# Optimization experiments

Measured on AMD Instinct MI355X. Metric: run time of the kernel, lower is better.

The kernel has to match this reference:

```python
import jax, jax.numpy as jnp
import numpy as np

COND = 128  # mask = first 128 dims are condition (True); last 128 are transformed


def _mlp(h, W1, b1, W2, b2, W3, b3):
    h = jax.nn.relu(h @ W1 + b1)
    h = jax.nn.relu(h @ W2 + b2)
    return h @ W3 + b3


def setup_inputs() -> dict:
    key = jax.random.key(0)
    ks = jax.random.split(key, 8)
    B, D, H, T = 65536, 256, 512, 128
    s = 0.02  # small init so exp(tanh(s_vals)) is well-behaved
    inp = {
        "x": jax.random.normal(ks[0], (B, D), dtype=jnp.float32),
        "Ws1": jax.random.normal(ks[1], (COND, H), dtype=jnp.float32) * s,
        "bs1": jnp.zeros((H,), jnp.float32),
        "Ws2": jax.random.normal(ks[2], (H, H), dtype=jnp.float32) * s,
        "bs2": jnp.zeros((H,), jnp.float32),
        "Ws3": jax.random.normal(ks[3], (H, T), dtype=jnp.float32) * s,
        "bs3": jnp.zeros((T,), jnp.float32),
        "Wt1": jax.random.normal(ks[4], (COND, H), dtype=jnp.float32) * s,
        "bt1": jnp.zeros((H,), jnp.float32),
        "Wt2": jax.random.normal(ks[5], (H, H), dtype=jnp.float32) * s,
        "bt2": jnp.zeros((H,), jnp.float32),
        "Wt3": jax.random.normal(ks[6], (H, T), dtype=jnp.float32) * s,
        "bt3": jnp.zeros((T,), jnp.float32),
    }
    return inp


def reference(x, Ws1, bs1, Ws2, bs2, Ws3, bs3, Wt1, bt1, Wt2, bt2, Wt3, bt3):
    # mask gather: condition = masked dims, transform = the rest
    cond = x[:, :COND]            # [B, COND]
    x_t = x[:, COND:]             # [B, T]
    s_vals = jnp.tanh(_mlp(cond, Ws1, bs1, Ws2, bs2, Ws3, bs3))  # [B, T]
    t_vals = _mlp(cond, Wt1, bt1, Wt2, bt2, Wt3, bt3)            # [B, T]
    y_partial = x_t * jnp.exp(s_vals) + t_vals                   # forward branch (inverse=False)
    log_det = s_vals.sum(axis=1)                                 # [B]
    y = jnp.concatenate([cond, y_partial], axis=1)               # scatter back
    return (y, log_det)
```

## Files before the change

kernel.cpp:

```cpp
#include <hip/hip_runtime.h>
#include <hip/hip_bf16.h>

typedef __bf16          bf16x8_t __attribute__((ext_vector_type(8)));
typedef float           f32x4_t  __attribute__((ext_vector_type(4)));
typedef unsigned short  u16x4_t  __attribute__((ext_vector_type(4)));

#define DIN      256
#define CONDN    128
#define BM       64
#define NTHREADS 1024
#define NWAVE    16
#define LDS_S    132

#define OFF_WS1 0
#define OFF_WS2 65536
#define OFF_WS3 327680
#define OFF_WT1 393216
#define OFF_WT2 458752
#define OFF_WT3 720896
#define W_TOTAL 786432

__global__ void prep_w(const float* __restrict__ Ws1, const float* __restrict__ Ws2,
                       const float* __restrict__ Ws3, const float* __restrict__ Wt1,
                       const float* __restrict__ Wt2, const float* __restrict__ Wt3,
                       __hip_bfloat16* __restrict__ wt) {
  int idx = blockIdx.x * blockDim.x + threadIdx.x;
  if (idx >= W_TOTAL) return;
  const float* W; int K, N, off;
  if (idx < OFF_WS2)      { W = Ws1; K = 128; N = 512; off = idx - OFF_WS1; }
  else if (idx < OFF_WS3) { W = Ws2; K = 512; N = 512; off = idx - OFF_WS2; }
  else if (idx < OFF_WT1) { W = Ws3; K = 512; N = 128; off = idx - OFF_WS3; }
  else if (idx < OFF_WT2) { W = Wt1; K = 128; N = 512; off = idx - OFF_WT1; }
  else if (idx < OFF_WT3) { W = Wt2; K = 512; N = 512; off = idx - OFF_WT2; }
  else                    { W = Wt3; K = 512; N = 128; off = idx - OFF_WT3; }
  int n = off / K;
  int k = off - n * K;
  wt[idx] = __float2bfloat16(W[k * N + n]);
}

#define SWZ(row, col) (((((col) >> 3) ^ ((row) & 7)) << 3) + ((col) & 7))

template<int KTOT, int LDB, int MTT, int NT>
__device__ __forceinline__ void mm_tile(const __hip_bfloat16* __restrict__ As, const int lda,
                                        const __hip_bfloat16* __restrict__ Bsrc,
                                        const int l15, const int l4, f32x4_t acc[MTT][NT]) {
  const int xr = l15 & 7;
  const __hip_bfloat16* bp = Bsrc + (size_t)l15 * LDB + l4 * 8;
  constexpr int NS = KTOT / 32;
  constexpr int DEPTH = (NS < 3) ? NS : 3;
  bf16x8_t ring[DEPTH][NT];
  bf16x8_t a[MTT];
  #pragma unroll
  for (int p = 0; p < DEPTH; ++p) {
    #pragma unroll
    for (int n = 0; n < NT; ++n)
      ring[p][n] = *reinterpret_cast<const bf16x8_t*>(bp + (size_t)n * 16 * LDB + p * 32);
  }
  #pragma unroll
  for (int s = 0; s < NS; ++s) {
    #pragma unroll
    for (int m = 0; m < MTT; ++m)
      a[m] = *reinterpret_cast<const bf16x8_t*>(
          &As[(m * 16 + l15) * lda + (((s * 4 + l4) ^ xr) << 3)]);
    #pragma unroll
    for (int m = 0; m < MTT; ++m) {
      #pragma unroll
      for (int n = 0; n < NT; ++n)
        acc[m][n] = __builtin_amdgcn_mfma_f32_16x16x32_bf16(a[m], ring[s % DEPTH][n], acc[m][n], 0, 0, 0);
    }
    if (s + DEPTH < NS) {
      #pragma unroll
      for (int n = 0; n < NT; ++n)
        ring[s % DEPTH][n] = *reinterpret_cast<const bf16x8_t*>(bp + (size_t)n * 16 * LDB + (s + DEPTH) * 32);
    }
  }
}

template<int MTT, int NT, int LD>
__device__ __forceinline__ void relu_store(f32x4_t acc[MTT][NT], const float* __restrict__ bias,
                                           const int n0, const int l15, const int l4,
                                           __hip_bfloat16* __restrict__ H) {
  #pragma unroll
  for (int n = 0; n < NT; ++n) {
    const int col = n0 + n * 16 + l15;
    const float bv = bias[col];
    #pragma unroll
    for (int m = 0; m < MTT; ++m) {
      #pragma unroll
      for (int r = 0; r < 4; ++r) {
        const int row = m * 16 + l4 * 4 + r;
        float v = fmaxf(acc[m][n][r] + bv, 0.0f);
        H[row * LD + SWZ(row, col)] = __float2bfloat16(v);
      }
    }
  }
}

#define ZERO_ACC(acc, MTT, NT) do {                       \
    _Pragma("unroll") for (int m_ = 0; m_ < MTT; ++m_)    \
    _Pragma("unroll") for (int n_ = 0; n_ < NT; ++n_)     \
      acc[m_][n_] = (f32x4_t){0.f, 0.f, 0.f, 0.f};        \
  } while (0)

__global__ __launch_bounds__(NTHREADS, 1)
void realnvp_fused(const float* __restrict__ x, const __hip_bfloat16* __restrict__ wt,
                   const float* __restrict__ bs1, const float* __restrict__ bs2,
                   const float* __restrict__ bs3, const float* __restrict__ bt1,
                   const float* __restrict__ bt2, const float* __restrict__ bt3,
                   float* __restrict__ y, float* __restrict__ ld) {
  __shared__ __hip_bfloat16 sA[BM * CONDN];
  __shared__ __hip_bfloat16 sH[BM * 512];
  __shared__ float sS[BM * LDS_S];
  __shared__ float tS[BM * LDS_S];
  float* sLd = reinterpret_cast<float*>(sA);

  const int tid  = threadIdx.x;
  const int lane = tid & 63;
  const int wid  = tid >> 6;
  const int l15  = lane & 15;
  const int l4   = lane >> 4;
  const int row0 = blockIdx.x * BM;
  const int n0   = wid * 32;
  const int g    = wid >> 3;
  const int wA   = wid & 7;
  const int n3   = wA * 16;

  #pragma unroll
  for (int i = 0; i < 2; ++i) {
    int f = tid + i * NTHREADS;
    int r = f >> 5;
    int c = (f & 31) << 2;
    const float4 v = *reinterpret_cast<const float4*>(&x[(size_t)(row0 + r) * DIN + c]);
    *reinterpret_cast<float4*>(&y[(size_t)(row0 + r) * DIN + c]) = v;
    union { u16x4_t u; __hip_bfloat16 b[4]; } p;
    p.b[0] = __float2bfloat16(v.x); p.b[1] = __float2bfloat16(v.y);
    p.b[2] = __float2bfloat16(v.z); p.b[3] = __float2bfloat16(v.w);
    *reinterpret_cast<u16x4_t*>(&sA[r * CONDN + SWZ(r, c)]) = p.u;
  }
  __syncthreads();

  f32x4_t acc[4][2];
  f32x4_t sfrag[4], tfrag[4];

  ZERO_ACC(acc, 4, 2);
  mm_tile<128, 128, 4, 2>(sA, CONDN, wt + OFF_WS1 + (size_t)n0 * 128, l15, l4, acc);
  relu_store<4, 2, 512>(acc, bs1, n0, l15, l4, sH);
  __syncthreads();
  ZERO_ACC(acc, 4, 2);
  mm_tile<512, 512, 4, 2>(sH, 512, wt + OFF_WS2 + (size_t)n0 * 512, l15, l4, acc);
  __syncthreads();
  relu_store<4, 2, 512>(acc, bs2, n0, l15, l4, sH);
  __syncthreads();
  {
    f32x4_t a3[4][1];
    ZERO_ACC(a3, 4, 1);
    mm_tile<256, 512, 4, 1>(sH + g * 256, 512,
                            wt + OFF_WS3 + (size_t)n3 * 512 + g * 256, l15, l4, a3);
    if (g == 0) {
      #pragma unroll
      for (int m = 0; m < 4; ++m) sfrag[m] = a3[m][0];
    } else {
      #pragma unroll
      for (int m = 0; m < 4; ++m)
        #pragma unroll
        for (int r = 0; r < 4; ++r)
          sS[(m * 16 + l4 * 4 + r) * LDS_S + n3 + l15] = a3[m][0][r];
    }
  }
  __syncthreads();

  ZERO_ACC(acc, 4, 2);
  mm_tile<128, 128, 4, 2>(sA, CONDN, wt + OFF_WT1 + (size_t)n0 * 128, l15, l4, acc);
  relu_store<4, 2, 512>(acc, bt1, n0, l15, l4, sH);
  __syncthreads();
  ZERO_ACC(acc, 4, 2);
  mm_tile<512, 512, 4, 2>(sH, 512, wt + OFF_WT2 + (size_t)n0 * 512, l15, l4, acc);
  __syncthreads();
  relu_store<4, 2, 512>(acc, bt2, n0, l15, l4, sH);
  __syncthreads();
  {
    f32x4_t a3[4][1];
    ZERO_ACC(a3, 4, 1);
    mm_tile<256, 512, 4, 1>(sH + g * 256, 512,
                            wt + OFF_WT3 + (size_t)n3 * 512 + g * 256, l15, l4, a3);
    if (g == 0) {
      #pragma unroll
      for (int m = 0; m < 4; ++m) tfrag[m] = a3[m][0];
    } else {
      #pragma unroll
      for (int m = 0; m < 4; ++m)
        #pragma unroll
        for (int r = 0; r < 4; ++r)
          tS[(m * 16 + l4 * 4 + r) * LDS_S + n3 + l15] = a3[m][0][r];
    }
  }
  __syncthreads();

  if (g == 0) {
    const float bsv = bs3[n3 + l15];
    const float btv = bt3[n3 + l15];
    #pragma unroll
    for (int m = 0; m < 4; ++m) {
      #pragma unroll
      for (int r = 0; r < 4; ++r) {
        const int rl   = m * 16 + l4 * 4 + r;
        const int grow = row0 + rl;
        const int col  = n3 + l15;
        float s = tanhf(sfrag[m][r] + sS[rl * LDS_S + col] + bsv);
        float t = tfrag[m][r] + tS[rl * LDS_S + col] + btv;
        float xv = x[(size_t)grow * DIN + CONDN + col];
        y[(size_t)grow * DIN + CONDN + col] = xv * expf(s) + t;
        float ss = s;
        ss += __shfl_xor(ss, 1);
        ss += __shfl_xor(ss, 2);
        ss += __shfl_xor(ss, 4);
        ss += __shfl_xor(ss, 8);
        if (l15 == 0) sLd[wA * BM + rl] = ss;
      }
    }
  }
  __syncthreads();
  if (tid < BM) {
    float v = 0.f;
    #pragma unroll
    for (int w = 0; w < 8; ++w) v += sLd[w * BM + tid];
    ld[row0 + tid] = v;
  }
}

extern "C" void kernel_launch(void* const* d_in, const int* in_sizes, int n_in,
                              void* d_out, int out_size, void* d_ws, size_t ws_size,
                              hipStream_t stream) {
  const float* x   = (const float*)d_in[0];
  const float* Ws1 = (const float*)d_in[1];
  const float* bs1 = (const float*)d_in[2];
  const float* Ws2 = (const float*)d_in[3];
  const float* bs2 = (const float*)d_in[4];
  const float* Ws3 = (const float*)d_in[5];
  const float* bs3 = (const float*)d_in[6];
  const float* Wt1 = (const float*)d_in[7];
  const float* bt1 = (const float*)d_in[8];
  const float* Wt2 = (const float*)d_in[9];
  const float* bt2 = (const float*)d_in[10];
  const float* Wt3 = (const float*)d_in[11];
  const float* bt3 = (const float*)d_in[12];

  const int Btot = in_sizes[0] / DIN;
  float* y  = (float*)d_out;
  float* ld = (float*)d_out + (size_t)Btot * DIN;
  __hip_bfloat16* wt = (__hip_bfloat16*)d_ws;

  prep_w<<<(W_TOTAL + 255) / 256, 256, 0, stream>>>(Ws1, Ws2, Ws3, Wt1, Wt2, Wt3, wt);
  realnvp_fused<<<Btot / BM, NTHREADS, 0, stream>>>(x, wt, bs1, bs2, bs3,
                                                    bt1, bt2, bt3, y, ld);
}
```

Measured before the change: 271.8 us.

## Split layer-3 GEMM by rows instead of K, drop LDS reduction buffers

```diff
diff --git a/kernel.cpp b/kernel.cpp
--- a/kernel.cpp
+++ b/kernel.cpp
@@ -10,7 +10,6 @@
 #define BM       64
 #define NTHREADS 1024
 #define NWAVE    16
-#define LDS_S    132
 
 #define OFF_WS1 0
 #define OFF_WS2 65536
@@ -47,7 +46,7 @@
   const int xr = l15 & 7;
   const __hip_bfloat16* bp = Bsrc + (size_t)l15 * LDB + l4 * 8;
   constexpr int NS = KTOT / 32;
-  constexpr int DEPTH = (NS < 3) ? NS : 3;
+  constexpr int DEPTH = (NS < 2) ? NS : 2;
   bf16x8_t ring[DEPTH][NT];
   bf16x8_t a[MTT];
   #pragma unroll
@@ -110,8 +109,6 @@
                    float* __restrict__ y, float* __restrict__ ld) {
   __shared__ __hip_bfloat16 sA[BM * CONDN];
   __shared__ __hip_bfloat16 sH[BM * 512];
-  __shared__ float sS[BM * LDS_S];
-  __shared__ float tS[BM * LDS_S];
   float* sLd = reinterpret_cast<float*>(sA);
 
   const int tid  = threadIdx.x;
@@ -121,9 +118,9 @@
   const int l4   = lane >> 4;
   const int row0 = blockIdx.x * BM;
   const int n0   = wid * 32;
-  const int g    = wid >> 3;
   const int wA   = wid & 7;
   const int n3   = wA * 16;
+  const int rb   = (wid >> 3) * 32;
 
   #pragma unroll
   for (int i = 0; i < 2; ++i) {
@@ -140,7 +137,7 @@
   __syncthreads();
 
   f32x4_t acc[4][2];
-  f32x4_t sfrag[4], tfrag[4];
+  f32x4_t sfrag[2], tfrag[2];
 
   ZERO_ACC(acc, 4, 2);
   mm_tile<128, 128, 4, 2>(sA, CONDN, wt + OFF_WS1 + (size_t)n0 * 128, l15, l4, acc);
@@ -152,20 +149,10 @@
   relu_store<4, 2, 512>(acc, bs2, n0, l15, l4, sH);
   __syncthreads();
   {
-    f32x4_t a3[4][1];
-    ZERO_ACC(a3, 4, 1);
-    mm_tile<256, 512, 4, 1>(sH + g * 256, 512,
-                            wt + OFF_WS3 + (size_t)n3 * 512 + g * 256, l15, l4, a3);
-    if (g == 0) {
-      #pragma unroll
-      for (int m = 0; m < 4; ++m) sfrag[m] = a3[m][0];
-    } else {
-      #pragma unroll
-      for (int m = 0; m < 4; ++m)
-        #pragma unroll
-        for (int r = 0; r < 4; ++r)
-          sS[(m * 16 + l4 * 4 + r) * LDS_S + n3 + l15] = a3[m][0][r];
-    }
+    f32x4_t a3[2][1];
+    ZERO_ACC(a3, 2, 1);
+    mm_tile<512, 512, 2, 1>(sH + rb * 512, 512, wt + OFF_WS3 + (size_t)n3 * 512, l15, l4, a3);
+    sfrag[0] = a3[0][0]; sfrag[1] = a3[1][0];
   }
   __syncthreads();
 
@@ -179,44 +166,31 @@
   relu_store<4, 2, 512>(acc, bt2, n0, l15, l4, sH);
   __syncthreads();
   {
-    f32x4_t a3[4][1];
-    ZERO_ACC(a3, 4, 1);
-    mm_tile<256, 512, 4, 1>(sH + g * 256, 512,
-                            wt + OFF_WT3 + (size_t)n3 * 512 + g * 256, l15, l4, a3);
-    if (g == 0) {
-      #pragma unroll
-      for (int m = 0; m < 4; ++m) tfrag[m] = a3[m][0];
-    } else {
-      #pragma unroll
-      for (int m = 0; m < 4; ++m)
-        #pragma unroll
-        for (int r = 0; r < 4; ++r)
-          tS[(m * 16 + l4 * 4 + r) * LDS_S + n3 + l15] = a3[m][0][r];
-    }
-  }
-  __syncthreads();
-
-  if (g == 0) {
-    const float bsv = bs3[n3 + l15];
-    const float btv = bt3[n3 + l15];
-    #pragma unroll
-    for (int m = 0; m < 4; ++m) {
-      #pragma unroll
-      for (int r = 0; r < 4; ++r) {
-        const int rl   = m * 16 + l4 * 4 + r;
-        const int grow = row0 + rl;
-        const int col  = n3 + l15;
-        float s = tanhf(sfrag[m][r] + sS[rl * LDS_S + col] + bsv);
-        float t = tfrag[m][r] + tS[rl * LDS_S + col] + btv;
-        float xv = x[(size_t)grow * DIN + CONDN + col];
-        y[(size_t)grow * DIN + CONDN + col] = xv * expf(s) + t;
-        float ss = s;
-        ss += __shfl_xor(ss, 1);
-        ss += __shfl_xor(ss, 2);
-        ss += __shfl_xor(ss, 4);
-        ss += __shfl_xor(ss, 8);
-        if (l15 == 0) sLd[wA * BM + rl] = ss;
-      }
+    f32x4_t a3[2][1];
+    ZERO_ACC(a3, 2, 1);
+    mm_tile<512, 512, 2, 1>(sH + rb * 512, 512, wt + OFF_WT3 + (size_t)n3 * 512, l15, l4, a3);
+    tfrag[0] = a3[0][0]; tfrag[1] = a3[1][0];
+  }
+
+  const float bsv = bs3[n3 + l15];
+  const float btv = bt3[n3 + l15];
+  #pragma unroll
+  for (int m = 0; m < 2; ++m) {
+    #pragma unroll
+    for (int r = 0; r < 4; ++r) {
+      const int rl   = rb + m * 16 + l4 * 4 + r;
+      const int grow = row0 + rl;
+      const int col  = n3 + l15;
+      float s = tanhf(sfrag[m][r] + bsv);
+      float t = tfrag[m][r] + btv;
+      float xv = x[(size_t)grow * DIN + CONDN + col];
+      y[(size_t)grow * DIN + CONDN + col] = xv * expf(s) + t;
+      float ss = s;
+      ss += __shfl_xor(ss, 1);
+      ss += __shfl_xor(ss, 2);
+      ss += __shfl_xor(ss, 4);
+      ss += __shfl_xor(ss, 8);
+      if (l15 == 0) sLd[wA * BM + rl] = ss;
     }
   }
   __syncthreads();
```

New measurement: 290.4 us. 6.9% more time.
